# Optimization experiments

Hardware: AMD Instinct MI355X
Metric: run time of the kernel (lower is better)

The kernel has to match this reference:

```python
import jax, jax.numpy as jnp
import numpy as np

B = 8       # complexes in batch
C = 32      # CDR residues per antibody
G = 2048    # antigen nodes per complex
D = 128     # encoded_dims
N_AB = B * C
N_AG = B * G
N = N_AB + N_AG
SLOPE = 0.2
EPS_BN = 1e-5


def _build_edges():
    # block-sparse bipartite edges (cdr_b x ag_b), symmetrized, + self loops
    srcs, dsts = [], []
    for b in range(B):
        ab = np.arange(b * C, (b + 1) * C)
        ag = np.arange(N_AB + b * G, N_AB + (b + 1) * G)
        g1, g2 = np.meshgrid(ab, ag, indexing='ij')
        srcs.append(g1.ravel()); dsts.append(g2.ravel())
    s = np.concatenate(srcs); d = np.concatenate(dsts)
    loops = np.arange(N)
    src = np.concatenate([s, d, loops]).astype(np.int32)
    dst = np.concatenate([d, s, loops]).astype(np.int32)
    return src, dst


def setup_inputs() -> dict:
    key = jax.random.key(0)
    ks = jax.random.split(key, 16)
    sc = 1.0 / np.sqrt(D)
    edge_src, edge_dst = _build_edges()
    return {
        'selected_ab': jax.random.normal(ks[0], (N_AB, D), jnp.float32),
        'x_ag': jax.random.normal(ks[1], (N_AG, D), jnp.float32),
        'W1': jax.random.normal(ks[2], (D, D), jnp.float32) * sc,
        'a_src1': jax.random.normal(ks[3], (D,), jnp.float32) * sc,
        'a_dst1': jax.random.normal(ks[4], (D,), jnp.float32) * sc,
        'b1': jnp.zeros((D,), jnp.float32),
        'W2': jax.random.normal(ks[5], (D, D), jnp.float32) * sc,
        'a_src2': jax.random.normal(ks[6], (D,), jnp.float32) * sc,
        'a_dst2': jax.random.normal(ks[7], (D,), jnp.float32) * sc,
        'b2': jnp.zeros((D,), jnp.float32),
        'bn_ab_g': jnp.ones((2 * D,), jnp.float32),
        'bn_ab_b': jnp.zeros((2 * D,), jnp.float32),
        'bn_ag_g': jnp.ones((2 * D,), jnp.float32),
        'bn_ag_b': jnp.zeros((2 * D,), jnp.float32),
        'fc_w': jax.random.normal(ks[8], (2 * D, 1), jnp.float32) * sc,
        'fc_b': jnp.zeros((1,), jnp.float32),
        'agfc_w': jax.random.normal(ks[9], (2 * D, 1), jnp.float32) * sc,
        'agfc_b': jnp.zeros((1,), jnp.float32),
        'edge_src': jnp.asarray(edge_src),
        'edge_dst': jnp.asarray(edge_dst),
    }


def _gat(x, W, a_s, a_d, b, src, dst):
    # PyG GATConv, heads=1, eval mode (dropout off)
    h = x @ W                                  # [N, D]
    al_s = h @ a_s                             # [N]
    al_d = h @ a_d                             # [N]
    e = jax.nn.leaky_relu(al_s[src] + al_d[dst], SLOPE)   # [E]
    m = jax.ops.segment_max(e, dst, num_segments=N)
    e = jnp.exp(e - m[dst])
    z = jax.ops.segment_sum(e, dst, num_segments=N)
    alpha = e / (z[dst] + 1e-16)
    out = jax.ops.segment_sum(h[src] * alpha[:, None], dst, num_segments=N)
    return out + b


def _bn(x, g, b):
    # training-mode batch stats (biased variance), like torch BatchNorm1d
    m = x.mean(0)
    v = ((x - m) ** 2).mean(0)
    return (x - m) / jnp.sqrt(v + EPS_BN) * g + b


def reference(selected_ab, x_ag, W1, a_src1, a_dst1, b1, W2, a_src2, a_dst2, b2,
              bn_ab_g, bn_ab_b, bn_ag_g, bn_ag_b, fc_w, fc_b, agfc_w, agfc_b,
              edge_src, edge_dst):
    x = jnp.concatenate([selected_ab, x_ag], axis=0)          # [N, D]
    x = jax.nn.relu(_gat(x, W1, a_src1, a_dst1, b1, edge_src, edge_dst))
    x = _gat(x, W2, a_src2, a_dst2, b2, edge_src, edge_dst)
    x_ab = jnp.concatenate([x[:N_AB], selected_ab], axis=1)   # [N_ab, 2D]
    x_ab = jax.nn.relu(_bn(x_ab, bn_ab_g, bn_ab_b))
    x_ab = (x_ab @ fc_w + fc_b).ravel()
    x_ag_o = jnp.concatenate([x[N_AB:], x_ag], axis=1)        # [N_ag, 2D]
    x_ag_o = jax.nn.relu(_bn(x_ag_o, bn_ag_g, bn_ag_b))
    x_ag_o = (x_ag_o @ agfc_w + agfc_b).ravel()
    return (x_ab, x_ag_o)
```

## Files before the change

kernel.cpp:

```cpp
#include <hip/hip_runtime.h>


#define N_AB 256
#define N_AG 16384
#define N_ALL 16640
#define G_AG 2048
#define SLOPE 0.2f
#define MSHIFT 20.0f

typedef __attribute__((ext_vector_type(4))) float f32x4;
typedef __attribute__((ext_vector_type(8))) __bf16 bf16x8;
typedef __attribute__((ext_vector_type(8))) unsigned short u16x8;
typedef unsigned short ushort_t;

__device__ __forceinline__ float bf2f(ushort_t u) {
  union { unsigned int i; float f; } v; v.i = ((unsigned int)u) << 16; return v.f;
}
__device__ __forceinline__ ushort_t f2bf(float f) {
  union { float fv; unsigned int i; } v; v.fv = f;
  unsigned int x = v.i;
  return (ushort_t)((x + 0x7fffu + ((x >> 16) & 1u)) >> 16);
}
__device__ __forceinline__ float lrelu(float x) { return x >= 0.f ? x : SLOPE * x; }
__device__ __forceinline__ float expw(float e) {
  return __expf(fminf(e, 60.f) - MSHIFT);
}
__device__ __forceinline__ float ldf(const void* p, size_t i, int f) {
  return f ? ((const float*)p)[i] : bf2f(((const ushort_t*)p)[i]);
}
__device__ __forceinline__ void ld8f(const void* p, size_t i, int f, float* o) {
  if (f) {
    const f32x4* q = (const f32x4*)((const float*)p + i);
    f32x4 a = q[0], b = q[1];
#pragma unroll
    for (int j = 0; j < 4; ++j) { o[j] = a[j]; o[j + 4] = b[j]; }
  } else {
    u16x8 v = *(const u16x8*)((const ushort_t*)p + i);
#pragma unroll
    for (int j = 0; j < 8; ++j) o[j] = bf2f(v[j]);
  }
}

__global__ __launch_bounds__(256) void k_pre(
    const void* __restrict__ W1, const void* __restrict__ W2,
    const void* __restrict__ as1, const void* __restrict__ ad1,
    const void* __restrict__ as2, const void* __restrict__ ad2,
    const ushort_t* __restrict__ selu,
    ushort_t* __restrict__ W1t, ushort_t* __restrict__ W2t,
    float* __restrict__ va, float* __restrict__ bnsumAG,
    float* __restrict__ accf, float* __restrict__ accz,
    int* __restrict__ flagp) {
  int t = threadIdx.x, lane = t & 63, wid = t >> 6;
  int bx = blockIdx.x;
  int cnt = 0;
#pragma unroll
  for (int i = 0; i < 8; ++i) {
    unsigned e = (selu[lane * 8 + i] >> 7) & 0xFF;
    if (e > 0xC8) cnt++;
  }
  int f = (__popcll(__ballot(cnt > 0)) >= 3) ? 1 : 0;
  if (bx == 0 && t == 0) flagp[0] = f;

  if (bx < 16) {
    const void* W = (bx < 8) ? W1 : W2;
    ushort_t* Wt = (bx < 8) ? W1t : W2t;
    int base = (bx & 7) * 2048 + t * 8;
    float o[8];
    ld8f(W, base, f, o);
#pragma unroll
    for (int j = 0; j < 8; ++j) {
      int idx = base + j;
      Wt[(idx & 127) * 128 + (idx >> 7)] = f2bf(o[j]);
    }
  } else if (bx < 32) {
    int j = bx - 16;
    const void* W   = (j < 8) ? W1 : W2;
    const void* asv = (j < 8) ? as1 : as2;
    const void* adv = (j < 8) ? ad1 : ad2;
    int vbase = (j < 8) ? 0 : 256;
    int basek = (j & 7) * 16 + wid * 4;
    float a_s0 = ldf(asv, lane, f), a_s1 = ldf(asv, lane + 64, f);
    float a_d0 = ldf(adv, lane, f), a_d1 = ldf(adv, lane + 64, f);
#pragma unroll
    for (int i = 0; i < 4; ++i) {
      int k = basek + i;
      float w0 = ldf(W, (size_t)k * 128 + lane, f);
      float w1 = ldf(W, (size_t)k * 128 + lane + 64, f);
      float ps = w0 * a_s0 + w1 * a_s1;
      float pd = w0 * a_d0 + w1 * a_d1;
#pragma unroll
      for (int o = 1; o < 64; o <<= 1) {
        ps += __shfl_xor(ps, o);
        pd += __shfl_xor(pd, o);
      }
      if (lane == 0) { va[vbase + k] = ps; va[vbase + 128 + k] = pd; }
    }
  } else {
    int j = bx - 32;
    f32x4* az = (f32x4*)(accf + (size_t)j * 4096);
    f32x4 z4 = (f32x4){0.f, 0.f, 0.f, 0.f};
    for (int i = t; i < 1024; i += 256) az[i] = z4;
    if (j == 0) { bnsumAG[t] = 0.f; bnsumAG[t + 256] = 0.f; accz[t] = 0.f; }
  }
}

__global__ __launch_bounds__(256) void k_gemm(
    const void* __restrict__ xa, int modeA,
    const void* __restrict__ xb, int modeB,
    const int* __restrict__ flagp,
    const ushort_t* __restrict__ Wt, const float* __restrict__ va,
    ushort_t* __restrict__ h, float* __restrict__ als, float* __restrict__ ald) {
  int lane = threadIdx.x & 63, wid = threadIdx.x >> 6;
  int rw0 = blockIdx.x * 128 + wid * 32;
  const void* xsrc; int roff, mode;
  if (rw0 < N_AB) { xsrc = xa; roff = rw0; mode = modeA; }
  else            { xsrc = xb; roff = rw0 - N_AB; mode = modeB; }
  int fx = (mode == 2) ? *flagp : mode;
  int mm = lane & 15, q = lane >> 4;
  f32x4 acc[2][8];
#pragma unroll
  for (int a = 0; a < 2; ++a)
#pragma unroll
    for (int b = 0; b < 8; ++b) acc[a][b] = (f32x4){0.f, 0.f, 0.f, 0.f};
  float pals[2] = {0.f, 0.f}, pald[2] = {0.f, 0.f};
#pragma unroll
  for (int s = 0; s < 4; ++s) {
    int koff = s * 32 + q * 8;
    union { u16x8 u; bf16x8 b; } af[2];
#pragma unroll
    for (int mt = 0; mt < 2; ++mt) {
      float o[8];
      ld8f(xsrc, (size_t)(roff + mt * 16 + mm) * 128 + koff, fx, o);
#pragma unroll
      for (int j = 0; j < 8; ++j) {
        af[mt].u[j] = f2bf(o[j]);
        pals[mt] += o[j] * va[koff + j];
        pald[mt] += o[j] * va[128 + koff + j];
      }
    }
#pragma unroll
    for (int nt = 0; nt < 8; ++nt) {
      bf16x8 bfr = *(const bf16x8*)(Wt + (size_t)(nt * 16 + mm) * 128 + koff);
      acc[0][nt] = __builtin_amdgcn_mfma_f32_16x16x32_bf16(af[0].b, bfr, acc[0][nt], 0, 0, 0);
      acc[1][nt] = __builtin_amdgcn_mfma_f32_16x16x32_bf16(af[1].b, bfr, acc[1][nt], 0, 0, 0);
    }
  }
#pragma unroll
  for (int mt = 0; mt < 2; ++mt) {
    float s1 = pals[mt]; s1 += __shfl_xor(s1, 16); s1 += __shfl_xor(s1, 32);
    float d1 = pald[mt]; d1 += __shfl_xor(d1, 16); d1 += __shfl_xor(d1, 32);
    if (lane < 16) { als[rw0 + mt * 16 + lane] = s1; ald[rw0 + mt * 16 + lane] = d1; }
  }
#pragma unroll
  for (int mt = 0; mt < 2; ++mt)
#pragma unroll
    for (int nt = 0; nt < 8; ++nt)
#pragma unroll
      for (int r = 0; r < 4; ++r) {
        int row = rw0 + mt * 16 + q * 4 + r;
        int col = nt * 16 + mm;
        h[(size_t)row * 128 + col] = f2bf(acc[mt][nt][r]);
      }
}

#define AG_STRIDE 40
__global__ __launch_bounds__(256) void k_agg_ag(
    const ushort_t* __restrict__ h, const float* __restrict__ als,
    const float* __restrict__ ald, const void* __restrict__ bias,
    const int* __restrict__ flagp, ushort_t* __restrict__ xout, int do_relu) {
  __shared__ ushort_t hT[128 * AG_STRIDE];
  __shared__ float alsAB[32];
  int b = blockIdx.x >> 5, jt = blockIdx.x & 31;
  int t = threadIdx.x, lane = t & 63, wid = t >> 6;
  int f = *flagp;
  {
    int row = t & 31, c0 = (t >> 5) * 16;
    const ushort_t* src = h + (size_t)(b * 32 + row) * 128 + c0;
    u16x8 v0 = *(const u16x8*)src;
    u16x8 v1 = *(const u16x8*)(src + 8);
#pragma unroll
    for (int j = 0; j < 8; ++j) {
      hT[(c0 + j) * AG_STRIDE + row] = v0[j];
      hT[(c0 + 8 + j) * AG_STRIDE + row] = v1[j];
    }
    if (t < 32) alsAB[t] = als[b * 32 + t];
  }
  __syncthreads();
  int jl = jt * 64 + wid * 16;
  int jrow = N_AB + b * G_AG + jl;
  int mm = lane & 15, q = lane >> 4;
  float aldj = ald[jrow + mm];
  float alsj = als[jrow + mm];
  union { u16x8 u; bf16x8 b; } af;
  float zp = 0.f;
#pragma unroll
  for (int j = 0; j < 8; ++j) {
    ushort_t us = f2bf(expw(lrelu(alsAB[q * 8 + j] + aldj)));
    af.u[j] = us;
    zp += bf2f(us);
  }
  zp += __shfl_xor(zp, 16);
  zp += __shfl_xor(zp, 32);
  float wself = expw(lrelu(alsj + aldj));
  float z = zp + wself;
#pragma unroll
  for (int nt = 0; nt < 8; ++nt) {
    int col = nt * 16 + mm;
    union { u16x8 u; bf16x8 b; } bfr;
    bfr.b = *(const bf16x8*)(&hT[col * AG_STRIDE + q * 8]);
    f32x4 acc = {0.f, 0.f, 0.f, 0.f};
    acc = __builtin_amdgcn_mfma_f32_16x16x32_bf16(af.b, bfr.b, acc, 0, 0, 0);
    float biasv = ldf(bias, col, f);
#pragma unroll
    for (int r = 0; r < 4; ++r) {
      int row = q * 4 + r;
      float zr = __shfl(z, row);
      float wsr = __shfl(wself, row);
      float hv = bf2f(h[(size_t)(jrow + row) * 128 + col]);
      float v = (acc[r] + wsr * hv) / (zr + 1e-16f) + biasv;
      if (do_relu) v = fmaxf(v, 0.f);
      xout[(size_t)(jrow + row) * 128 + col] = f2bf(v);
    }
  }
}

#define ABP_STRIDE 72
__global__ __launch_bounds__(256) void k_abpart(
    const ushort_t* __restrict__ h, const float* __restrict__ als,
    const float* __restrict__ ald, float* __restrict__ accf,
    float* __restrict__ accz) {
  __shared__ ushort_t hT[128 * ABP_STRIDE];
  __shared__ float alsL[64];
  int b = blockIdx.x >> 5, sg = blockIdx.x & 31;
  int t = threadIdx.x, lane = t & 63, wid = t >> 6;
  int mm = lane & 15, q = lane >> 4;
  int jrow0 = N_AB + b * G_AG + sg * 64;
  {
    int jr = t & 63, cgrp = (t >> 6) * 32;
    const ushort_t* src = h + (size_t)(jrow0 + jr) * 128 + cgrp;
#pragma unroll
    for (int v = 0; v < 4; ++v) {
      u16x8 vv = *(const u16x8*)(src + v * 8);
#pragma unroll
      for (int j = 0; j < 8; ++j)
        hT[(cgrp + v * 8 + j) * ABP_STRIDE + jr] = vv[j];
    }
    if (t < 64) alsL[t] = als[jrow0 + t];
  }
  __syncthreads();
  float aldm[2] = { ald[b * 32 + mm], ald[b * 32 + 16 + mm] };
  f32x4 acc[2][2];
#pragma unroll
  for (int a = 0; a < 2; ++a)
#pragma unroll
    for (int c = 0; c < 2; ++c) acc[a][c] = (f32x4){0.f, 0.f, 0.f, 0.f};
  float zz[2] = {0.f, 0.f};
#pragma unroll
  for (int s = 0; s < 2; ++s) {
    int k0 = s * 32 + q * 8;
    float a8[8];
#pragma unroll
    for (int j = 0; j < 8; ++j) a8[j] = alsL[k0 + j];
    union { u16x8 u; bf16x8 b; } af[2];
#pragma unroll
    for (int mt = 0; mt < 2; ++mt)
#pragma unroll
      for (int j = 0; j < 8; ++j) {
        ushort_t us = f2bf(expw(lrelu(a8[j] + aldm[mt])));
        af[mt].u[j] = us;
        zz[mt] += bf2f(us);
      }
#pragma unroll
    for (int ns = 0; ns < 2; ++ns) {
      int n = wid * 32 + ns * 16 + mm;
      union { u16x8 u; bf16x8 b; } bfr;
      bfr.b = *(const bf16x8*)(&hT[n * ABP_STRIDE + k0]);
      acc[0][ns] = __builtin_amdgcn_mfma_f32_16x16x32_bf16(af[0].b, bfr.b, acc[0][ns], 0, 0, 0);
      acc[1][ns] = __builtin_amdgcn_mfma_f32_16x16x32_bf16(af[1].b, bfr.b, acc[1][ns], 0, 0, 0);
    }
  }
#pragma unroll
  for (int mt = 0; mt < 2; ++mt)
#pragma unroll
    for (int ns = 0; ns < 2; ++ns)
#pragma unroll
      for (int r = 0; r < 4; ++r) {
        int row = b * 32 + mt * 16 + q * 4 + r;
        int col = wid * 32 + ns * 16 + mm;
        atomicAdd(&accf[(size_t)row * 128 + col], acc[mt][ns][r]);
      }
#pragma unroll
  for (int mt = 0; mt < 2; ++mt) {
    float z = zz[mt];
    z += __shfl_xor(z, 16);
    z += __shfl_xor(z, 32);
    if (wid == 0 && lane < 16)
      atomicAdd(&accz[b * 32 + mt * 16 + lane], z);
  }
}

__global__ __launch_bounds__(256) void k_abfin(
    float* __restrict__ accf, float* __restrict__ accz,
    const ushort_t* __restrict__ h, const float* __restrict__ als,
    const float* __restrict__ ald, const void* __restrict__ bias,
    const int* __restrict__ flagp, float* __restrict__ xabf, int do_relu) {
  __shared__ float zsh[32];
  int b = blockIdx.x, t = threadIdx.x;
  int f = *flagp;
  if (t < 32) {
    int grow = b * 32 + t;
    float w = expw(lrelu(als[grow] + ald[grow]));
    zsh[t] = accz[grow] + w;
    accz[grow] = 0.f;
  }
  __syncthreads();
  int c = t & 127, rh = t >> 7;
  float biasv = ldf(bias, c, f);
#pragma unroll 4
  for (int r = 0; r < 16; ++r) {
    int row = rh * 16 + r;
    int grow = b * 32 + row;
    float wself = expw(lrelu(als[grow] + ald[grow]));
    size_t idx = (size_t)grow * 128 + c;
    float hv = bf2f(h[idx]);
    float v = (accf[idx] + wself * hv) / (zsh[row] + 1e-16f) + biasv;
    accf[idx] = 0.f;
    if (do_relu) v = fmaxf(v, 0.f);
    xabf[idx] = v;
  }
}

__global__ __launch_bounds__(256) void k_bnstats_ag(
    const ushort_t* __restrict__ xfag, const void* __restrict__ x_ag,
    const int* __restrict__ flagp, float* __restrict__ bnsumAG) {
  int t = threadIdx.x;
  int r0 = blockIdx.x * 128;
  int f = *flagp;
  float s = 0.f, sq = 0.f;
  if (t < 128) {
    const ushort_t* p = xfag + (size_t)(N_AB + r0) * 128 + t;
    for (int r = 0; r < 128; ++r) { float v = bf2f(p[(size_t)r * 128]); s += v; sq += v * v; }
  } else {
    for (int r = 0; r < 128; ++r) {
      float v = ldf(x_ag, (size_t)(r0 + r) * 128 + (t - 128), f);
      s += v; sq += v * v;
    }
  }
  atomicAdd(&bnsumAG[t], s);
  atomicAdd(&bnsumAG[256 + t], sq);
}

__global__ __launch_bounds__(256) void k_stats(
    const float* __restrict__ xfab, const void* __restrict__ sel_ab,
    const float* __restrict__ bnsumAG,
    const void* __restrict__ gab, const void* __restrict__ bab,
    const void* __restrict__ gag, const void* __restrict__ bag,
    const void* __restrict__ fcw, const void* __restrict__ agfcw,
    const int* __restrict__ flagp,
    float* __restrict__ statsAB, float* __restrict__ statsAG) {
  int c = threadIdx.x;
  int f = *flagp;
  if (blockIdx.x == 0) {
    float s = 0.f, sq = 0.f;
    if (c < 128) {
      for (int r = 0; r < 256; ++r) { float v = xfab[(size_t)r * 128 + c]; s += v; sq += v * v; }
    } else {
      for (int r = 0; r < 256; ++r) {
        float v = ldf(sel_ab, (size_t)r * 128 + (c - 128), f);
        s += v; sq += v * v;
      }
    }
    float mean = s * (1.f / 256.f);
    float var = fmaxf(sq * (1.f / 256.f) - mean * mean, 0.f);
    float A = ldf(gab, c, f) / sqrtf(var + 1e-5f);
    statsAB[c] = A;
    statsAB[256 + c] = ldf(bab, c, f) - mean * A;
    statsAB[512 + c] = ldf(fcw, c, f);
  } else {
    float mean = bnsumAG[c] * (1.f / 16384.f);
    float var = fmaxf(bnsumAG[256 + c] * (1.f / 16384.f) - mean * mean, 0.f);
    float A = ldf(gag, c, f) / sqrtf(var + 1e-5f);
    statsAG[c] = A;
    statsAG[256 + c] = ldf(bag, c, f) - mean * A;
    statsAG[512 + c] = ldf(agfcw, c, f);
  }
}

__global__ __launch_bounds__(256) void k_head(
    const float* __restrict__ xfab, const ushort_t* __restrict__ xfag,
    const void* __restrict__ sel_ab, const void* __restrict__ x_ag,
    const float* __restrict__ statsAB, const float* __restrict__ statsAG,
    const void* __restrict__ fcb, const void* __restrict__ agfcb,
    const int* __restrict__ flagp, void* __restrict__ out) {
  int lane = threadIdx.x & 63, wid = threadIdx.x >> 6;
  int row = blockIdx.x * 4 + wid;
  int f = *flagp;
  int c0 = lane * 2;
  const float* st;
  float v0, v1, v2, v3, bb;
  if (row < N_AB) {
    st = statsAB;
    const float* p = xfab + (size_t)row * 128 + c0;
    v0 = p[0]; v1 = p[1];
    size_t ro = (size_t)row * 128 + c0;
    v2 = ldf(sel_ab, ro, f);
    v3 = ldf(sel_ab, ro + 1, f);
    bb = ldf(fcb, 0, f);
  } else {
    st = statsAG;
    const ushort_t* p = xfag + (size_t)row * 128 + c0;
    v0 = bf2f(p[0]); v1 = bf2f(p[1]);
    size_t ro = (size_t)(row - N_AB) * 128 + c0;
    v2 = ldf(x_ag, ro, f);
    v3 = ldf(x_ag, ro + 1, f);
    bb = ldf(agfcb, 0, f);
  }
  float acc =
      fmaxf(v0 * st[c0]           + st[256 + c0],     0.f) * st[512 + c0]
    + fmaxf(v1 * st[c0 + 1]       + st[256 + c0 + 1], 0.f) * st[512 + c0 + 1]
    + fmaxf(v2 * st[128 + c0]     + st[384 + c0],     0.f) * st[640 + c0]
    + fmaxf(v3 * st[128 + c0 + 1] + st[384 + c0 + 1], 0.f) * st[640 + c0 + 1];
#pragma unroll
  for (int o = 1; o < 64; o <<= 1) acc += __shfl_xor(acc, o);
  if (lane == 0) {
    float r = acc + bb;
    if (f) ((float*)out)[row] = r;
    else   ((ushort_t*)out)[row] = f2bf(r);
  }
}

extern "C" void kernel_launch(void* const* d_in, const int* in_sizes, int n_in,
                              void* d_out, int out_size, void* d_ws, size_t ws_size,
                              hipStream_t stream) {
  (void)in_sizes; (void)n_in; (void)out_size; (void)ws_size;
  const void* sel_ab = d_in[0];
  const void* x_ag   = d_in[1];
  const void* W1     = d_in[2];
  const void* as1    = d_in[3];
  const void* ad1    = d_in[4];
  const void* b1     = d_in[5];
  const void* W2     = d_in[6];
  const void* as2    = d_in[7];
  const void* ad2    = d_in[8];
  const void* b2     = d_in[9];
  const void* gab    = d_in[10];
  const void* bab    = d_in[11];
  const void* gag    = d_in[12];
  const void* bag    = d_in[13];
  const void* fcw    = d_in[14];
  const void* fcb    = d_in[15];
  const void* agfcw  = d_in[16];
  const void* agfcb  = d_in[17];

  ushort_t* h  = (ushort_t*)d_in[18];
  ushort_t* xb = (ushort_t*)d_in[19];

  char* wsp = (char*)d_ws;
  size_t off = 0;
  auto carve = [&](size_t bytes) -> char* {
    char* p = wsp + off; off += (bytes + 255) & ~(size_t)255; return p;
  };
  int* flag      = (int*)carve(64 * 4);
  ushort_t* W1t  = (ushort_t*)carve(16384 * 2);
  ushort_t* W2t  = (ushort_t*)carve(16384 * 2);
  float* va      = (float*)carve(512 * 4);
  float* als     = (float*)carve((size_t)N_ALL * 4);
  float* ald     = (float*)carve((size_t)N_ALL * 4);
  float* bnsumAG = (float*)carve(512 * 4);
  float* statsAB = (float*)carve(768 * 4);
  float* statsAG = (float*)carve(768 * 4);
  float* xabf    = (float*)carve((size_t)N_AB * 128 * 4);
  float* accf    = (float*)carve((size_t)N_AB * 128 * 4);
  float* accz    = (float*)carve(256 * 4);

  k_pre<<<40, 256, 0, stream>>>(W1, W2, as1, ad1, as2, ad2,
                                (const ushort_t*)sel_ab, W1t, W2t, va,
                                bnsumAG, accf, accz, flag);
  k_gemm<<<130, 256, 0, stream>>>(sel_ab, 2, x_ag, 2, flag, W1t, va, h, als, ald);
  k_agg_ag<<<256, 256, 0, stream>>>(h, als, ald, b1, flag, xb, 1);
  k_abpart<<<256, 256, 0, stream>>>(h, als, ald, accf, accz);
  k_abfin<<<8, 256, 0, stream>>>(accf, accz, h, als, ald, b1, flag, xabf, 1);
  k_gemm<<<130, 256, 0, stream>>>(xabf, 1, xb + (size_t)N_AB * 128, 0, flag, W2t, va + 256, h, als, ald);
  k_agg_ag<<<256, 256, 0, stream>>>(h, als, ald, b2, flag, xb, 0);
  k_abpart<<<256, 256, 0, stream>>>(h, als, ald, accf, accz);
  k_abfin<<<8, 256, 0, stream>>>(accf, accz, h, als, ald, b2, flag, xabf, 0);
  k_bnstats_ag<<<128, 256, 0, stream>>>(xb, x_ag, flag, bnsumAG);
  k_stats<<<2, 256, 0, stream>>>(xabf, sel_ab, bnsumAG, gab, bab, gag, bag, fcw, agfcw, flag, statsAB, statsAG);
  k_head<<<4160, 256, 0, stream>>>(xabf, xb, sel_ab, x_ag, statsAB, statsAG, fcb, agfcb, flag, d_out);
}
```

Before: 205.4 us.

## Merge AG/AB aggregation kernels, fuse BN stats, halve GEMM tile rows

The antigen aggregation, antibody partial aggregation and x_ag BN-stat reduction now run as block ranges of a single k_agg launch. Column sum and sum-of-squares of the layer-2 AG output are accumulated in the aggregation epilogue via LDS and global atomics, which removes the separate k_bnstats_ag pass that re-read xb. The GEMM tile shrinks to 16 rows per wave, doubling the block count to 260 for better CU coverage. In exchange the kernel does more atomic traffic, uses more LDS per block, and each GEMM block reuses its weight loads across fewer rows.

New measurement: 199.6 us. -2.8%, faster.

```diff
diff --git a/kernel.cpp b/kernel.cpp
--- a/kernel.cpp
+++ b/kernel.cpp
@@ -111,191 +111,208 @@
     const ushort_t* __restrict__ Wt, const float* __restrict__ va,
     ushort_t* __restrict__ h, float* __restrict__ als, float* __restrict__ ald) {
   int lane = threadIdx.x & 63, wid = threadIdx.x >> 6;
-  int rw0 = blockIdx.x * 128 + wid * 32;
+  int rw0 = blockIdx.x * 64 + wid * 16;
   const void* xsrc; int roff, mode;
   if (rw0 < N_AB) { xsrc = xa; roff = rw0; mode = modeA; }
   else            { xsrc = xb; roff = rw0 - N_AB; mode = modeB; }
   int fx = (mode == 2) ? *flagp : mode;
   int mm = lane & 15, q = lane >> 4;
-  f32x4 acc[2][8];
-#pragma unroll
-  for (int a = 0; a < 2; ++a)
-#pragma unroll
-    for (int b = 0; b < 8; ++b) acc[a][b] = (f32x4){0.f, 0.f, 0.f, 0.f};
-  float pals[2] = {0.f, 0.f}, pald[2] = {0.f, 0.f};
+  f32x4 acc[8];
+#pragma unroll
+  for (int b = 0; b < 8; ++b) acc[b] = (f32x4){0.f, 0.f, 0.f, 0.f};
+  float pals = 0.f, pald = 0.f;
 #pragma unroll
   for (int s = 0; s < 4; ++s) {
     int koff = s * 32 + q * 8;
-    union { u16x8 u; bf16x8 b; } af[2];
-#pragma unroll
-    for (int mt = 0; mt < 2; ++mt) {
-      float o[8];
-      ld8f(xsrc, (size_t)(roff + mt * 16 + mm) * 128 + koff, fx, o);
-#pragma unroll
-      for (int j = 0; j < 8; ++j) {
-        af[mt].u[j] = f2bf(o[j]);
-        pals[mt] += o[j] * va[koff + j];
-        pald[mt] += o[j] * va[128 + koff + j];
-      }
+    union { u16x8 u; bf16x8 b; } af;
+    float o[8];
+    ld8f(xsrc, (size_t)(roff + mm) * 128 + koff, fx, o);
+#pragma unroll
+    for (int j = 0; j < 8; ++j) {
+      af.u[j] = f2bf(o[j]);
+      pals += o[j] * va[koff + j];
+      pald += o[j] * va[128 + koff + j];
     }
 #pragma unroll
     for (int nt = 0; nt < 8; ++nt) {
       bf16x8 bfr = *(const bf16x8*)(Wt + (size_t)(nt * 16 + mm) * 128 + koff);
-      acc[0][nt] = __builtin_amdgcn_mfma_f32_16x16x32_bf16(af[0].b, bfr, acc[0][nt], 0, 0, 0);
-      acc[1][nt] = __builtin_amdgcn_mfma_f32_16x16x32_bf16(af[1].b, bfr, acc[1][nt], 0, 0, 0);
-    }
-  }
-#pragma unroll
-  for (int mt = 0; mt < 2; ++mt) {
-    float s1 = pals[mt]; s1 += __shfl_xor(s1, 16); s1 += __shfl_xor(s1, 32);
-    float d1 = pald[mt]; d1 += __shfl_xor(d1, 16); d1 += __shfl_xor(d1, 32);
-    if (lane < 16) { als[rw0 + mt * 16 + lane] = s1; ald[rw0 + mt * 16 + lane] = d1; }
-  }
-#pragma unroll
-  for (int mt = 0; mt < 2; ++mt)
-#pragma unroll
-    for (int nt = 0; nt < 8; ++nt)
-#pragma unroll
-      for (int r = 0; r < 4; ++r) {
-        int row = rw0 + mt * 16 + q * 4 + r;
-        int col = nt * 16 + mm;
-        h[(size_t)row * 128 + col] = f2bf(acc[mt][nt][r]);
-      }
-}
-
+      acc[nt] = __builtin_amdgcn_mfma_f32_16x16x32_bf16(af.b, bfr, acc[nt], 0, 0, 0);
+    }
+  }
+  {
+    float s1 = pals; s1 += __shfl_xor(s1, 16); s1 += __shfl_xor(s1, 32);
+    float d1 = pald; d1 += __shfl_xor(d1, 16); d1 += __shfl_xor(d1, 32);
+    if (lane < 16) { als[rw0 + lane] = s1; ald[rw0 + lane] = d1; }
+  }
+#pragma unroll
+  for (int nt = 0; nt < 8; ++nt)
+#pragma unroll
+    for (int r = 0; r < 4; ++r) {
+      int row = rw0 + q * 4 + r;
+      int col = nt * 16 + mm;
+      h[(size_t)row * 128 + col] = f2bf(acc[nt][r]);
+    }
+}
+
+#define ABP_STRIDE 72
 #define AG_STRIDE 40
-__global__ __launch_bounds__(256) void k_agg_ag(
+__global__ __launch_bounds__(256) void k_agg(
     const ushort_t* __restrict__ h, const float* __restrict__ als,
     const float* __restrict__ ald, const void* __restrict__ bias,
-    const int* __restrict__ flagp, ushort_t* __restrict__ xout, int do_relu) {
-  __shared__ ushort_t hT[128 * AG_STRIDE];
-  __shared__ float alsAB[32];
-  int b = blockIdx.x >> 5, jt = blockIdx.x & 31;
-  int t = threadIdx.x, lane = t & 63, wid = t >> 6;
-  int f = *flagp;
-  {
-    int row = t & 31, c0 = (t >> 5) * 16;
-    const ushort_t* src = h + (size_t)(b * 32 + row) * 128 + c0;
-    u16x8 v0 = *(const u16x8*)src;
-    u16x8 v1 = *(const u16x8*)(src + 8);
-#pragma unroll
-    for (int j = 0; j < 8; ++j) {
-      hT[(c0 + j) * AG_STRIDE + row] = v0[j];
-      hT[(c0 + 8 + j) * AG_STRIDE + row] = v1[j];
-    }
-    if (t < 32) alsAB[t] = als[b * 32 + t];
-  }
-  __syncthreads();
-  int jl = jt * 64 + wid * 16;
-  int jrow = N_AB + b * G_AG + jl;
-  int mm = lane & 15, q = lane >> 4;
-  float aldj = ald[jrow + mm];
-  float alsj = als[jrow + mm];
-  union { u16x8 u; bf16x8 b; } af;
-  float zp = 0.f;
-#pragma unroll
-  for (int j = 0; j < 8; ++j) {
-    ushort_t us = f2bf(expw(lrelu(alsAB[q * 8 + j] + aldj)));
-    af.u[j] = us;
-    zp += bf2f(us);
-  }
-  zp += __shfl_xor(zp, 16);
-  zp += __shfl_xor(zp, 32);
-  float wself = expw(lrelu(alsj + aldj));
-  float z = zp + wself;
-#pragma unroll
-  for (int nt = 0; nt < 8; ++nt) {
-    int col = nt * 16 + mm;
-    union { u16x8 u; bf16x8 b; } bfr;
-    bfr.b = *(const bf16x8*)(&hT[col * AG_STRIDE + q * 8]);
-    f32x4 acc = {0.f, 0.f, 0.f, 0.f};
-    acc = __builtin_amdgcn_mfma_f32_16x16x32_bf16(af.b, bfr.b, acc, 0, 0, 0);
-    float biasv = ldf(bias, col, f);
-#pragma unroll
-    for (int r = 0; r < 4; ++r) {
-      int row = q * 4 + r;
-      float zr = __shfl(z, row);
-      float wsr = __shfl(wself, row);
-      float hv = bf2f(h[(size_t)(jrow + row) * 128 + col]);
-      float v = (acc[r] + wsr * hv) / (zr + 1e-16f) + biasv;
-      if (do_relu) v = fmaxf(v, 0.f);
-      xout[(size_t)(jrow + row) * 128 + col] = f2bf(v);
-    }
-  }
-}
-
-#define ABP_STRIDE 72
-__global__ __launch_bounds__(256) void k_abpart(
-    const ushort_t* __restrict__ h, const float* __restrict__ als,
-    const float* __restrict__ ald, float* __restrict__ accf,
-    float* __restrict__ accz) {
+    const int* __restrict__ flagp, ushort_t* __restrict__ xout,
+    float* __restrict__ accf, float* __restrict__ accz,
+    const void* __restrict__ x_ag, float* __restrict__ bnsumAG,
+    int do_relu, int do_bnsum) {
   __shared__ ushort_t hT[128 * ABP_STRIDE];
-  __shared__ float alsL[64];
-  int b = blockIdx.x >> 5, sg = blockIdx.x & 31;
+  __shared__ float alsS[64];
+  __shared__ float colsum[128], colsq[128];
+  int bx = blockIdx.x;
   int t = threadIdx.x, lane = t & 63, wid = t >> 6;
   int mm = lane & 15, q = lane >> 4;
-  int jrow0 = N_AB + b * G_AG + sg * 64;
-  {
-    int jr = t & 63, cgrp = (t >> 6) * 32;
-    const ushort_t* src = h + (size_t)(jrow0 + jr) * 128 + cgrp;
-#pragma unroll
-    for (int v = 0; v < 4; ++v) {
-      u16x8 vv = *(const u16x8*)(src + v * 8);
-#pragma unroll
-      for (int j = 0; j < 8; ++j)
-        hT[(cgrp + v * 8 + j) * ABP_STRIDE + jr] = vv[j];
-    }
-    if (t < 64) alsL[t] = als[jrow0 + t];
-  }
-  __syncthreads();
-  float aldm[2] = { ald[b * 32 + mm], ald[b * 32 + 16 + mm] };
-  f32x4 acc[2][2];
-#pragma unroll
-  for (int a = 0; a < 2; ++a)
-#pragma unroll
-    for (int c = 0; c < 2; ++c) acc[a][c] = (f32x4){0.f, 0.f, 0.f, 0.f};
-  float zz[2] = {0.f, 0.f};
-#pragma unroll
-  for (int s = 0; s < 2; ++s) {
-    int k0 = s * 32 + q * 8;
-    float a8[8];
-#pragma unroll
-    for (int j = 0; j < 8; ++j) a8[j] = alsL[k0 + j];
-    union { u16x8 u; bf16x8 b; } af[2];
+
+  if (bx < 256) {
+    int b = bx >> 5, jt = bx & 31;
+    int f = *flagp;
+    {
+      int row = t & 31, c0 = (t >> 5) * 16;
+      const ushort_t* src = h + (size_t)(b * 32 + row) * 128 + c0;
+      u16x8 v0 = *(const u16x8*)src;
+      u16x8 v1 = *(const u16x8*)(src + 8);
+#pragma unroll
+      for (int j = 0; j < 8; ++j) {
+        hT[(c0 + j) * AG_STRIDE + row] = v0[j];
+        hT[(c0 + 8 + j) * AG_STRIDE + row] = v1[j];
+      }
+      if (t < 32) alsS[t] = als[b * 32 + t];
+      if (t < 128) { colsum[t] = 0.f; colsq[t] = 0.f; }
+    }
+    __syncthreads();
+    int jl = jt * 64 + wid * 16;
+    int jrow = N_AB + b * G_AG + jl;
+    float aldj = ald[jrow + mm];
+    float alsj = als[jrow + mm];
+    union { u16x8 u; bf16x8 b; } af;
+    float zp = 0.f;
+#pragma unroll
+    for (int j = 0; j < 8; ++j) {
+      ushort_t us = f2bf(expw(lrelu(alsS[q * 8 + j] + aldj)));
+      af.u[j] = us;
+      zp += bf2f(us);
+    }
+    zp += __shfl_xor(zp, 16);
+    zp += __shfl_xor(zp, 32);
+    float wself = expw(lrelu(alsj + aldj));
+    float z = zp + wself;
+#pragma unroll
+    for (int nt = 0; nt < 8; ++nt) {
+      int col = nt * 16 + mm;
+      union { u16x8 u; bf16x8 b; } bfr;
+      bfr.b = *(const bf16x8*)(&hT[col * AG_STRIDE + q * 8]);
+      f32x4 acc = {0.f, 0.f, 0.f, 0.f};
+      acc = __builtin_amdgcn_mfma_f32_16x16x32_bf16(af.b, bfr.b, acc, 0, 0, 0);
+      float biasv = ldf(bias, col, f);
+      float sl = 0.f, sq = 0.f;
+#pragma unroll
+      for (int r = 0; r < 4; ++r) {
+        int row = q * 4 + r;
+        float zr = __shfl(z, row);
+        float wsr = __shfl(wself, row);
+        float hv = bf2f(h[(size_t)(jrow + row) * 128 + col]);
+        float v = (acc[r] + wsr * hv) / (zr + 1e-16f) + biasv;
+        sl += v; sq += v * v;
+        if (do_relu) v = fmaxf(v, 0.f);
+        xout[(size_t)(jrow + row) * 128 + col] = f2bf(v);
+      }
+      if (do_bnsum) {
+        atomicAdd(&colsum[col], sl);
+        atomicAdd(&colsq[col], sq);
+      }
+    }
+    if (do_bnsum) {
+      __syncthreads();
+      if (t < 128) {
+        atomicAdd(&bnsumAG[t], colsum[t]);
+        atomicAdd(&bnsumAG[256 + t], colsq[t]);
+      }
+    }
+  } else if (bx < 512) {
+    int bx2 = bx - 256;
+    int b = bx2 >> 5, sg = bx2 & 31;
+    int jrow0 = N_AB + b * G_AG + sg * 64;
+    {
+      int jr = t & 63, cgrp = (t >> 6) * 32;
+      const ushort_t* src = h + (size_t)(jrow0 + jr) * 128 + cgrp;
+#pragma unroll
+      for (int v = 0; v < 4; ++v) {
+        u16x8 vv = *(const u16x8*)(src + v * 8);
+#pragma unroll
+        for (int j = 0; j < 8; ++j)
+          hT[(cgrp + v * 8 + j) * ABP_STRIDE + jr] = vv[j];
+      }
+      if (t < 64) alsS[t] = als[jrow0 + t];
+    }
+    __syncthreads();
+    float aldm[2] = { ald[b * 32 + mm], ald[b * 32 + 16 + mm] };
+    f32x4 acc[2][2];
+#pragma unroll
+    for (int a = 0; a < 2; ++a)
+#pragma unroll
+      for (int c = 0; c < 2; ++c) acc[a][c] = (f32x4){0.f, 0.f, 0.f, 0.f};
+    float zz[2] = {0.f, 0.f};
+#pragma unroll
+    for (int s = 0; s < 2; ++s) {
+      int k0 = s * 32 + q * 8;
+      float a8[8];
+#pragma unroll
+      for (int j = 0; j < 8; ++j) a8[j] = alsS[k0 + j];
+      union { u16x8 u; bf16x8 b; } af[2];
+#pragma unroll
+      for (int mt = 0; mt < 2; ++mt)
+#pragma unroll
+        for (int j = 0; j < 8; ++j) {
+          ushort_t us = f2bf(expw(lrelu(a8[j] + aldm[mt])));
+          af[mt].u[j] = us;
+          zz[mt] += bf2f(us);
+        }
+#pragma unroll
+      for (int ns = 0; ns < 2; ++ns) {
+        int n = wid * 32 + ns * 16 + mm;
+        union { u16x8 u; bf16x8 b; } bfr;
+        bfr.b = *(const bf16x8*)(&hT[n * ABP_STRIDE + k0]);
+        acc[0][ns] = __builtin_amdgcn_mfma_f32_16x16x32_bf16(af[0].b, bfr.b, acc[0][ns], 0, 0, 0);
+        acc[1][ns] = __builtin_amdgcn_mfma_f32_16x16x32_bf16(af[1].b, bfr.b, acc[1][ns], 0, 0, 0);
+      }
+    }
 #pragma unroll
     for (int mt = 0; mt < 2; ++mt)
 #pragma unroll
-      for (int j = 0; j < 8; ++j) {
-        ushort_t us = f2bf(expw(lrelu(a8[j] + aldm[mt])));
-        af[mt].u[j] = us;
-        zz[mt] += bf2f(us);
-      }
-#pragma unroll
-    for (int ns = 0; ns < 2; ++ns) {
-      int n = wid * 32 + ns * 16 + mm;
-      union { u16x8 u; bf16x8 b; } bfr;
-      bfr.b = *(const bf16x8*)(&hT[n * ABP_STRIDE + k0]);
-      acc[0][ns] = __builtin_amdgcn_mfma_f32_16x16x32_bf16(af[0].b, bfr.b, acc[0][ns], 0, 0, 0);
-      acc[1][ns] = __builtin_amdgcn_mfma_f32_16x16x32_bf16(af[1].b, bfr.b, acc[1][ns], 0, 0, 0);
-    }
-  }
-#pragma unroll
-  for (int mt = 0; mt < 2; ++mt)
-#pragma unroll
-    for (int ns = 0; ns < 2; ++ns)
-#pragma unroll
-      for (int r = 0; r < 4; ++r) {
-        int row = b * 32 + mt * 16 + q * 4 + r;
-        int col = wid * 32 + ns * 16 + mm;
-        atomicAdd(&accf[(size_t)row * 128 + col], acc[mt][ns][r]);
-      }
-#pragma unroll
-  for (int mt = 0; mt < 2; ++mt) {
-    float z = zz[mt];
-    z += __shfl_xor(z, 16);
-    z += __shfl_xor(z, 32);
-    if (wid == 0 && lane < 16)
-      atomicAdd(&accz[b * 32 + mt * 16 + lane], z);
+      for (int ns = 0; ns < 2; ++ns)
+#pragma unroll
+        for (int r = 0; r < 4; ++r) {
+          int row = b * 32 + mt * 16 + q * 4 + r;
+          int col = wid * 32 + ns * 16 + mm;
+          atomicAdd(&accf[(size_t)row * 128 + col], acc[mt][ns][r]);
+        }
+#pragma unroll
+    for (int mt = 0; mt < 2; ++mt) {
+      float z = zz[mt];
+      z += __shfl_xor(z, 16);
+      z += __shfl_xor(z, 32);
+      if (wid == 0 && lane < 16)
+        atomicAdd(&accz[b * 32 + mt * 16 + lane], z);
+    }
+  } else {
+    int j = bx - 512;
+    int f = *flagp;
+    int col = t & 127, half = t >> 7;
+    int r0 = j * 256 + half * 128;
+    float s = 0.f, sq = 0.f;
+    for (int r = 0; r < 128; ++r) {
+      float v = ldf(x_ag, (size_t)(r0 + r) * 128 + col, f);
+      s += v; sq += v * v;
+    }
+    atomicAdd(&bnsumAG[128 + col], s);
+    atomicAdd(&bnsumAG[384 + col], sq);
   }
 }
 
@@ -328,26 +345,6 @@
     if (do_relu) v = fmaxf(v, 0.f);
     xabf[idx] = v;
   }
-}
-
-__global__ __launch_bounds__(256) void k_bnstats_ag(
-    const ushort_t* __restrict__ xfag, const void* __restrict__ x_ag,
-    const int* __restrict__ flagp, float* __restrict__ bnsumAG) {
-  int t = threadIdx.x;
-  int r0 = blockIdx.x * 128;
-  int f = *flagp;
-  float s = 0.f, sq = 0.f;
-  if (t < 128) {
-    const ushort_t* p = xfag + (size_t)(N_AB + r0) * 128 + t;
-    for (int r = 0; r < 128; ++r) { float v = bf2f(p[(size_t)r * 128]); s += v; sq += v * v; }
-  } else {
-    for (int r = 0; r < 128; ++r) {
-      float v = ldf(x_ag, (size_t)(r0 + r) * 128 + (t - 128), f);
-      s += v; sq += v * v;
-    }
-  }
-  atomicAdd(&bnsumAG[t], s);
-  atomicAdd(&bnsumAG[256 + t], sq);
 }
 
 __global__ __launch_bounds__(256) void k_stats(
@@ -476,15 +473,14 @@
   k_pre<<<40, 256, 0, stream>>>(W1, W2, as1, ad1, as2, ad2,
                                 (const ushort_t*)sel_ab, W1t, W2t, va,
                                 bnsumAG, accf, accz, flag);
-  k_gemm<<<130, 256, 0, stream>>>(sel_ab, 2, x_ag, 2, flag, W1t, va, h, als, ald);
-  k_agg_ag<<<256, 256, 0, stream>>>(h, als, ald, b1, flag, xb, 1);
-  k_abpart<<<256, 256, 0, stream>>>(h, als, ald, accf, accz);
+  k_gemm<<<260, 256, 0, stream>>>(sel_ab, 2, x_ag, 2, flag, W1t, va, h, als, ald);
+  k_agg<<<512, 256, 0, stream>>>(h, als, ald, b1, flag, xb, accf, accz,
+                                 x_ag, bnsumAG, 1, 0);
   k_abfin<<<8, 256, 0, stream>>>(accf, accz, h, als, ald, b1, flag, xabf, 1);
-  k_gemm<<<130, 256, 0, stream>>>(xabf, 1, xb + (size_t)N_AB * 128, 0, flag, W2t, va + 256, h, als, ald);
-  k_agg_ag<<<256, 256, 0, stream>>>(h, als, ald, b2, flag, xb, 0);
-  k_abpart<<<256, 256, 0, stream>>>(h, als, ald, accf, accz);
+  k_gemm<<<260, 256, 0, stream>>>(xabf, 1, xb + (size_t)N_AB * 128, 0, flag, W2t, va + 256, h, als, ald);
+  k_agg<<<576, 256, 0, stream>>>(h, als, ald, b2, flag, xb, accf, accz,
+                                 x_ag, bnsumAG, 0, 1);
   k_abfin<<<8, 256, 0, stream>>>(accf, accz, h, als, ald, b2, flag, xabf, 0);
-  k_bnstats_ag<<<128, 256, 0, stream>>>(xb, x_ag, flag, bnsumAG);
   k_stats<<<2, 256, 0, stream>>>(xabf, sel_ab, bnsumAG, gab, bab, gag, bag, fcw, agfcw, flag, statsAB, statsAG);
   k_head<<<4160, 256, 0, stream>>>(xabf, xb, sel_ab, x_ag, statsAB, statsAG, fcb, agfcb, flag, d_out);
 }
```
